# Performance work log

Hardware: AMD Instinct MI355X
Metric: run time of the kernel (lower is better)

Reference implementation:

```python
import jax, jax.numpy as jnp
import numpy as np

N_NODES = 10000
N_EDGES = 100000
IN_CH = 384
PROJ = 768  # in_channels * projection_factor
N_BLOCKS = 4
OUT_CH = 128
LN_EPS = 1e-5


def _p(key, shape, fan_in):
    return jax.random.normal(key, shape, dtype=jnp.float32) * (1.0 / np.sqrt(fan_in))


def setup_inputs() -> dict:
    key = jax.random.key(0)
    ks = iter(jax.random.split(key, 64))
    x = jax.random.normal(next(ks), (N_NODES, IN_CH), dtype=jnp.float32)
    edge_index = jax.random.randint(next(ks), (2, N_EDGES), 0, N_NODES, dtype=jnp.int64)
    inp = {
        'x': x,
        'edge_index': edge_index,
        'proj_W': _p(next(ks), (PROJ, IN_CH), IN_CH),
        'proj_b': jnp.zeros((PROJ,), jnp.float32),
        'norm_w': jnp.ones((N_BLOCKS, PROJ), jnp.float32),
        'norm_b': jnp.zeros((N_BLOCKS, PROJ), jnp.float32),
        'g1_W': _p(next(ks), (N_BLOCKS, 4 * 192, PROJ), PROJ),
        'g1_as': _p(next(ks), (N_BLOCKS, 4, 192), 192),
        'g1_ad': _p(next(ks), (N_BLOCKS, 4, 192), 192),
        'g1_b': jnp.zeros((N_BLOCKS, 4 * 192), jnp.float32),
        'g2_W': _p(next(ks), (N_BLOCKS, 2 * 96, PROJ), PROJ),
        'g2_as': _p(next(ks), (N_BLOCKS, 2, 96), 96),
        'g2_ad': _p(next(ks), (N_BLOCKS, 2, 96), 96),
        'g2_b': jnp.zeros((N_BLOCKS, 2 * 96), jnp.float32),
        'uni_W': _p(next(ks), (N_BLOCKS, PROJ, 960), 960),
        'uni_b': jnp.zeros((N_BLOCKS, PROJ), jnp.float32),
        'fnorm_w': jnp.ones((PROJ,), jnp.float32),
        'fnorm_b': jnp.zeros((PROJ,), jnp.float32),
        'fg_W': _p(next(ks), (8 * OUT_CH, PROJ), PROJ),
        'fg_as': _p(next(ks), (8, OUT_CH), OUT_CH),
        'fg_ad': _p(next(ks), (8, OUT_CH), OUT_CH),
        'fg_b': jnp.zeros((OUT_CH,), jnp.float32),
    }
    return inp


def layer_norm(x, w, b):
    m = x.mean(-1, keepdims=True)
    v = ((x - m) ** 2).mean(-1, keepdims=True)
    return (x - m) / jnp.sqrt(v + LN_EPS) * w + b


def gat_conv(x, src, dst, W, a_src, a_dst, bias, heads, out_ch, concat):
    # PyG GATConv (eval mode, add_self_loops already applied in src/dst).
    n = x.shape[0]
    h = (x @ W.T).reshape(n, heads, out_ch)          # [N,H,C]
    al_s = jnp.einsum('nhc,hc->nh', h, a_src)        # [N,H]
    al_d = jnp.einsum('nhc,hc->nh', h, a_dst)
    e = jax.nn.leaky_relu(al_s[src] + al_d[dst], 0.2)  # [E,H]
    emax = jax.ops.segment_max(e, dst, num_segments=n)
    ee = jnp.exp(e - emax[dst])
    den = jax.ops.segment_sum(ee, dst, num_segments=n)
    alpha = ee / (den[dst] + 1e-16)                  # softmax over incoming edges
    out = jax.ops.segment_sum(h[src] * alpha[:, :, None], dst, num_segments=n)
    out = out.reshape(n, heads * out_ch) if concat else out.mean(axis=1)
    return out + bias


def reference(x, edge_index, proj_W, proj_b, norm_w, norm_b,
              g1_W, g1_as, g1_ad, g1_b, g2_W, g2_as, g2_ad, g2_b,
              uni_W, uni_b, fnorm_w, fnorm_b, fg_W, fg_as, fg_ad, fg_b):
    n = x.shape[0]
    loop = jnp.arange(n, dtype=edge_index.dtype)
    src = jnp.concatenate([edge_index[0], loop])  # add self loops (PyG default)
    dst = jnp.concatenate([edge_index[1], loop])

    h = jax.nn.elu(x @ proj_W.T + proj_b)
    for i in range(N_BLOCKS):
        res = h
        hn = layer_norm(h, norm_w[i], norm_b[i])
        o1 = gat_conv(hn, src, dst, g1_W[i], g1_as[i], g1_ad[i], g1_b[i], 4, 192, True)
        o2 = gat_conv(hn, src, dst, g2_W[i], g2_as[i], g2_ad[i], g2_b[i], 2, 96, True)
        cat = jax.nn.elu(jnp.concatenate([o1, o2], axis=-1))  # [N,960]
        h = jax.nn.elu(res + cat @ uni_W[i].T + uni_b[i])
    h = layer_norm(h, fnorm_w, fnorm_b)
    return gat_conv(h, src, dst, fg_W, fg_as, fg_ad, fg_b, 8, OUT_CH, False)
```

## Files before the change

### kernel.cpp

```cpp
#include <hip/hip_runtime.h>
#include <math.h>

#define N_NODES 10000
#define N_EDGES 100000
#define E_TOT   (N_EDGES + N_NODES)
#define PROJ    768
#define LN_EPS  1e-5f

typedef __attribute__((ext_vector_type(8))) short bf16x8;
typedef __attribute__((ext_vector_type(4))) short bf16x4;
typedef __attribute__((ext_vector_type(4))) float f32x4;

__device__ __forceinline__ float elu_f(float x){ return x > 0.f ? x : __expf(x) - 1.f; }
__device__ __forceinline__ float bf2f(unsigned short u){ return __uint_as_float(((unsigned int)u) << 16); }
__device__ __forceinline__ unsigned short f2bf(float f){
  unsigned int u = __float_as_uint(f);
  return (unsigned short)((u + 0x7FFFu + ((u >> 16) & 1u)) >> 16);
}

#define GLOAD16(gp, lp) __builtin_amdgcn_global_load_lds((const __attribute__((address_space(1))) void*)(gp), (__attribute__((address_space(3))) void*)(lp), 16, 0, 0)

__global__ void k_count(const int* __restrict__ ei, int* __restrict__ cnt){
  int e = blockIdx.x*blockDim.x + threadIdx.x;
  if (e >= E_TOT) return;
  int dst = (e < N_EDGES) ? ei[N_EDGES + e] : (e - N_EDGES);
  atomicAdd(&cnt[dst], 1);
}

__global__ void k_scan(const int* __restrict__ cnt, int* __restrict__ indptr, int* __restrict__ pos){
  __shared__ int s[1024];
  __shared__ int s_running;
  int t = threadIdx.x;
  if (t == 0) s_running = 0;
  __syncthreads();
  for (int base = 0; base < N_NODES; base += 1024){
    int v = (base + t < N_NODES) ? cnt[base + t] : 0;
    s[t] = v; __syncthreads();
    for (int off = 1; off < 1024; off <<= 1){
      int add = (t >= off) ? s[t - off] : 0;
      __syncthreads();
      s[t] += add;
      __syncthreads();
    }
    int total = s[1023];
    int run = s_running;
    if (base + t < N_NODES){
      int val = run + s[t] - v;
      indptr[base + t] = val;
      pos[base + t] = val;
    }
    __syncthreads();
    if (t == 0) s_running = run + total;
    __syncthreads();
  }
  if (t == 0) indptr[N_NODES] = s_running;
}

__global__ void k_fill(const int* __restrict__ ei, int* __restrict__ pos,
                       int* __restrict__ csr_src){
  int e = blockIdx.x*blockDim.x + threadIdx.x;
  if (e >= E_TOT) return;
  int s, d;
  if (e < N_EDGES){ s = ei[e]; d = ei[N_EDGES + e]; }
  else            { s = d = e - N_EDGES; }
  int p = atomicAdd(&pos[d], 1);
  csr_src[p] = s;
}

__global__ void k_f2bf_multi(const float4* __restrict__ s0, ushort4* __restrict__ d0, int n0,
                             const float4* __restrict__ s1, ushort4* __restrict__ d1, int n1,
                             const float4* __restrict__ s2, ushort4* __restrict__ d2, int n2,
                             const float4* __restrict__ s3, ushort4* __restrict__ d3, int n3){
  int i = blockIdx.x*blockDim.x + threadIdx.x;
  const float4* src; ushort4* dst; int idx;
  if (i < n0){ src = s0; dst = d0; idx = i; }
  else if (i < n0+n1){ src = s1; dst = d1; idx = i-n0; }
  else if (i < n0+n1+n2){ src = s2; dst = d2; idx = i-n0-n1; }
  else if (i < n0+n1+n2+n3){ src = s3; dst = d3; idx = i-n0-n1-n2; }
  else return;
  float4 v = src[idx];
  ushort4 o;
  o.x = f2bf(v.x); o.y = f2bf(v.y); o.z = f2bf(v.z); o.w = f2bf(v.w);
  dst[idx] = o;
}

__global__ void k_pack_l1l2(const float* __restrict__ g1, const float* __restrict__ g2,
                            unsigned short* __restrict__ dst){
  int i = blockIdx.x*blockDim.x + threadIdx.x;
  if (i >= 737280) return;
  int layer = i / 184320;
  int off4  = i - layer*184320;
  float4 v;
  if (off4 < 147456) v = *((const float4*)(g1 + (size_t)layer*589824) + off4);
  else               v = *((const float4*)(g2 + (size_t)layer*147456) + (off4 - 147456));
  ushort4 o;
  o.x = f2bf(v.x); o.y = f2bf(v.y); o.z = f2bf(v.z); o.w = f2bf(v.w);
  ((ushort4*)(dst + (size_t)layer*737280))[off4] = o;
}

__global__ void k_layernorm_bf(const unsigned short* __restrict__ x, const float* __restrict__ w,
                               const float* __restrict__ b, unsigned short* __restrict__ y){
  int n = blockIdx.x;
  int t = threadIdx.x;
  const unsigned short* xr = x + (size_t)n*PROJ;
  float v0=0.f, v1=0.f, v2=0.f, v3=0.f;
  if (t < 192){
    bf16x4 hv = *(const bf16x4*)(xr + t*4);
    v0 = bf2f((unsigned short)hv.x); v1 = bf2f((unsigned short)hv.y);
    v2 = bf2f((unsigned short)hv.z); v3 = bf2f((unsigned short)hv.w);
  }
  float s  = v0+v1+v2+v3;
  float s2 = v0*v0 + v1*v1 + v2*v2 + v3*v3;
  #pragma unroll
  for (int off = 32; off; off >>= 1){ s += __shfl_down(s, off); s2 += __shfl_down(s2, off); }
  __shared__ float rs[4], rs2[4];
  __shared__ float s_mean, s_rstd;
  int wid = t >> 6, lane = t & 63;
  if (lane == 0){ rs[wid] = s; rs2[wid] = s2; }
  __syncthreads();
  if (t == 0){
    float S  = rs[0]+rs[1]+rs[2]+rs[3];
    float S2 = rs2[0]+rs2[1]+rs2[2]+rs2[3];
    float m  = S * (1.f/768.f);
    float var = S2 * (1.f/768.f) - m*m;
    s_mean = m; s_rstd = rsqrtf(var + LN_EPS);
  }
  __syncthreads();
  if (t < 192){
    float m = s_mean, r = s_rstd;
    float4 wv = *(const float4*)&w[t*4];
    float4 bv = *(const float4*)&b[t*4];
    ushort4 o;
    o.x = f2bf((v0-m)*r*wv.x + bv.x);
    o.y = f2bf((v1-m)*r*wv.y + bv.y);
    o.z = f2bf((v2-m)*r*wv.z + bv.z);
    o.w = f2bf((v3-m)*r*wv.w + bv.w);
    *(ushort4*)(y + (size_t)n*PROJ + t*4) = o;
  }
}

template<int EPI>
__global__ __launch_bounds__(256, 8)
void k_gemm_mfma(const unsigned short* __restrict__ A, int lda,
                 const unsigned short* __restrict__ W,
                 unsigned short* __restrict__ C, int ldc,
                 int M, int N, int K,
                 const float* __restrict__ bias,
                 const unsigned short* __restrict__ res, int ldres, int NBN){
  __shared__ unsigned short As[3][128*32];
  __shared__ unsigned short Bs[3][64*32];
  const int tid = threadIdx.x;
  const int lane = tid & 63, wid = tid >> 6;
  const int wm = wid >> 1, wn = wid & 1;

  const int nwg = gridDim.x;
  const int q = nwg >> 3, r = nwg & 7;
  const int xcd = blockIdx.x & 7, o = blockIdx.x >> 3;
  const int swz = (xcd < r ? xcd*(q+1) : r*(q+1) + (xcd - r)*q) + o;
  const int bm = (swz / NBN) * 128;
  const int bn = (swz % NBN) * 64;

  const int srow = tid >> 2;
  const int sc   = (tid & 3) ^ ((tid >> 3) & 3);
  size_t ga0 = (size_t)min(bm + srow,      M-1)*lda + sc*8;
  size_t ga1 = (size_t)min(bm + 64 + srow, M-1)*lda + sc*8;
  size_t gb0 = (size_t)min(bn + srow,      N-1)*K   + sc*8;
  const int ldst = tid*8;

  f32x4 acc[4][2];
  #pragma unroll
  for (int i=0;i<4;i++)
    #pragma unroll
    for (int j=0;j<2;j++) acc[i][j] = (f32x4){0.f,0.f,0.f,0.f};

  const int rA = wm*64 + (lane & 15);
  const int rB = wn*32 + (lane & 15);
  const int cu = (((lane >> 4)) ^ (((lane & 15) >> 1) & 3)) * 8;

  const int NT = K >> 5;
  int bcur = 0;
  GLOAD16(A + ga0, &As[0][ldst]);
  GLOAD16(A + ga1, &As[0][2048 + ldst]);
  GLOAD16(W + gb0, &Bs[0][ldst]);

  for (int t = 0; t < NT; ++t){
    if (t + 1 < NT){
      int bst = bcur + 1; if (bst == 3) bst = 0;
      const int k0 = (t+1) << 5;
      GLOAD16(A + ga0 + k0, &As[bst][ldst]);
      GLOAD16(A + ga1 + k0, &As[bst][2048 + ldst]);
      GLOAD16(W + gb0 + k0, &Bs[bst][ldst]);
      asm volatile("s_waitcnt vmcnt(3)" ::: "memory");
    } else {
      asm volatile("s_waitcnt vmcnt(0)" ::: "memory");
    }
    __builtin_amdgcn_sched_barrier(0);
    __builtin_amdgcn_s_barrier();
    __builtin_amdgcn_sched_barrier(0);

    bf16x8 af[4], bfr[2];
    #pragma unroll
    for (int mi = 0; mi < 4; mi++)
      af[mi] = *(const bf16x8*)&As[bcur][(rA + mi*16)*32 + cu];
    #pragma unroll
    for (int ni = 0; ni < 2; ni++)
      bfr[ni] = *(const bf16x8*)&Bs[bcur][(rB + ni*16)*32 + cu];
    #pragma unroll
    for (int mi = 0; mi < 4; mi++)
      #pragma unroll
      for (int ni = 0; ni < 2; ni++)
        acc[mi][ni] = __builtin_amdgcn_mfma_f32_16x16x32_bf16(af[mi], bfr[ni], acc[mi][ni], 0,0,0);

    bcur += 1; if (bcur == 3) bcur = 0;
  }

  const int mrow0 = bm + wm*64 + ((lane>>4)<<2);
  const int ncol0 = bn + wn*32 + (lane & 15);
  #pragma unroll
  for (int mi=0; mi<4; mi++){
    #pragma unroll
    for (int rr=0; rr<4; rr++){
      int m = mrow0 + mi*16 + rr;
      if (m >= M) continue;
      #pragma unroll
      for (int ni=0; ni<2; ni++){
        int n = ncol0 + ni*16;
        float v = acc[mi][ni][rr];
        if (EPI == 1){
          v = elu_f(v + bias[n]);
        } else if (EPI == 2){
          v = elu_f(v + bias[n] + bf2f(res[(size_t)m*ldres + n]));
        }
        C[(size_t)m*ldc + n] = f2bf(v);
      }
    }
  }
}

__global__ void k_attn_coef6(const unsigned short* __restrict__ hlin,
                             const float* __restrict__ as1, const float* __restrict__ ad1,
                             const float* __restrict__ as2, const float* __restrict__ ad2,
                             float* __restrict__ als, float* __restrict__ ald){
  int n = blockIdx.x;
  int wid = threadIdx.x >> 6, lane = threadIdx.x & 63;
  int C    = wid < 4 ? 192 : 96;
  int base = wid < 4 ? wid*192 : 768 + (wid-4)*96;
  const float* as_ = wid < 4 ? as1 + wid*192 : as2 + (wid-4)*96;
  const float* ad_ = wid < 4 ? ad1 + wid*192 : ad2 + (wid-4)*96;
  float ss = 0.f, sd = 0.f;
  if (lane*4 < C){
    bf16x4 hv = *(const bf16x4*)(hlin + (size_t)n*960 + base + lane*4);
    float4 a1 = *(const float4*)&as_[lane*4];
    float4 a2 = *(const float4*)&ad_[lane*4];
    float h0 = bf2f((unsigned short)hv.x), h1 = bf2f((unsigned short)hv.y);
    float h2 = bf2f((unsigned short)hv.z), h3 = bf2f((unsigned short)hv.w);
    ss = h0*a1.x + h1*a1.y + h2*a1.z + h3*a1.w;
    sd = h0*a2.x + h1*a2.y + h2*a2.z + h3*a2.w;
  }
  #pragma unroll
  for (int off = 32; off; off >>= 1){ ss += __shfl_down(ss, off); sd += __shfl_down(sd, off); }
  if (lane == 0){ als[n*6 + wid] = ss; ald[n*6 + wid] = sd; }
}

__global__ void k_attn_coef8(const unsigned short* __restrict__ hlin,
                             const float* __restrict__ a_src, const float* __restrict__ a_dst,
                             float* __restrict__ als, float* __restrict__ ald){
  int n = blockIdx.x;
  int wid = threadIdx.x >> 6, lane = threadIdx.x & 63;
  float ss = 0.f, sd = 0.f;
  if (lane < 32){
    bf16x4 hv = *(const bf16x4*)(hlin + (size_t)n*1024 + wid*128 + lane*4);
    float4 a1 = *(const float4*)&a_src[wid*128 + lane*4];
    float4 a2 = *(const float4*)&a_dst[wid*128 + lane*4];
    float h0 = bf2f((unsigned short)hv.x), h1 = bf2f((unsigned short)hv.y);
    float h2 = bf2f((unsigned short)hv.z), h3 = bf2f((unsigned short)hv.w);
    ss = h0*a1.x + h1*a1.y + h2*a1.z + h3*a1.w;
    sd = h0*a2.x + h1*a2.y + h2*a2.z + h3*a2.w;
  }
  #pragma unroll
  for (int off = 32; off; off >>= 1){ ss += __shfl_down(ss, off); sd += __shfl_down(sd, off); }
  if (lane == 0){ als[n*8 + wid] = ss; ald[n*8 + wid] = sd; }
}

template<int MODE>
__global__ __launch_bounds__(256)
void k_attn_fused(const unsigned short* __restrict__ hlin, int ldh,
                  const float* __restrict__ als, const float* __restrict__ ald,
                  const int* __restrict__ indptr, const int* __restrict__ csr_src,
                  const float* __restrict__ b1, const float* __restrict__ b2,
                  void* __restrict__ outv, int ldo){
  constexpr int TOT = MODE ? 1024 : 960;
  constexpr int HT  = MODE ? 8 : 6;
  constexpr int CH8 = TOT/8;
  constexpr int CPL = (CH8 + 63)/64;
  int n = blockIdx.x;
  int tid = threadIdx.x;
  int wv = tid >> 6, lane = tid & 63;
  int beg = indptr[n], end = indptr[n+1], deg = end - beg;

  __shared__ float s_m[HT], s_dinv[HT], s_ald[HT];
  __shared__ float s_alpha[64*HT];
  __shared__ int   s_src[64];
  __shared__ float s_red[4][TOT];

  for (int h = wv; h < HT; h += 4){
    float aldv = ald[n*HT + h];
    float m = -1e30f, d = 0.f;
    for (int e = beg + lane; e < end; e += 64){
      int s = csr_src[e];
      float v = als[s*HT + h] + aldv;
      v = v > 0.f ? v : 0.2f*v;
      if (v > m){ d *= __expf(m - v); m = v; }
      d += __expf(v - m);
    }
    #pragma unroll
    for (int off = 1; off < 64; off <<= 1){
      float mo_ = __shfl_xor(m, off);
      float dd  = __shfl_xor(d, off);
      float mn  = fmaxf(m, mo_);
      d = d*__expf(m - mn) + dd*__expf(mo_ - mn);
      m = mn;
    }
    if (lane == 0){ s_m[h] = m; s_dinv[h] = 1.f/(d + 1e-16f); s_ald[h] = aldv; }
  }

  int hof[CPL];
  #pragma unroll
  for (int p = 0; p < CPL; p++){
    int idx = (lane + p*64)*8;
    hof[p] = MODE ? (idx >> 7) : (idx < 768 ? idx/192 : 4 + (idx-768)/96);
  }

  f32x4 accA[CPL], accB[CPL];
  #pragma unroll
  for (int p = 0; p < CPL; p++){ accA[p] = (f32x4){0,0,0,0}; accB[p] = (f32x4){0,0,0,0}; }

  for (int base = 0; base < deg; base += 64){
    int chunk = min(64, deg - base);
    __syncthreads();
    if (tid < chunk) s_src[tid] = csr_src[beg + base + tid];
    __syncthreads();
    for (int i = tid; i < chunk*HT; i += 256){
      int e = i / HT, h = i - e*HT;
      float v = als[s_src[e]*HT + h] + s_ald[h];
      v = v > 0.f ? v : 0.2f*v;
      s_alpha[e*HT + h] = __expf(v - s_m[h]) * s_dinv[h];
    }
    __syncthreads();

    int e = wv;
    for (; e + 4 < chunk; e += 8){
      int s0 = s_src[e], s1 = s_src[e+4];
      const bf16x8* hr0 = (const bf16x8*)(hlin + (size_t)s0*ldh);
      const bf16x8* hr1 = (const bf16x8*)(hlin + (size_t)s1*ldh);
      const float* ae0 = &s_alpha[e*HT];
      const float* ae1 = &s_alpha[(e+4)*HT];
      bf16x8 hv0[CPL], hv1[CPL];
      #pragma unroll
      for (int p = 0; p < CPL; p++){
        int ch = lane + p*64;
        if (CH8 % 64 == 0 || ch < CH8){ hv0[p] = hr0[ch]; hv1[p] = hr1[ch]; }
      }
      #pragma unroll
      for (int p = 0; p < CPL; p++){
        int ch = lane + p*64;
        if (CH8 % 64 == 0 || ch < CH8){
          float a0 = ae0[hof[p]], a1 = ae1[hof[p]];
          accA[p].x += bf2f((unsigned short)hv0[p][0])*a0 + bf2f((unsigned short)hv1[p][0])*a1;
          accA[p].y += bf2f((unsigned short)hv0[p][1])*a0 + bf2f((unsigned short)hv1[p][1])*a1;
          accA[p].z += bf2f((unsigned short)hv0[p][2])*a0 + bf2f((unsigned short)hv1[p][2])*a1;
          accA[p].w += bf2f((unsigned short)hv0[p][3])*a0 + bf2f((unsigned short)hv1[p][3])*a1;
          accB[p].x += bf2f((unsigned short)hv0[p][4])*a0 + bf2f((unsigned short)hv1[p][4])*a1;
          accB[p].y += bf2f((unsigned short)hv0[p][5])*a0 + bf2f((unsigned short)hv1[p][5])*a1;
          accB[p].z += bf2f((unsigned short)hv0[p][6])*a0 + bf2f((unsigned short)hv1[p][6])*a1;
          accB[p].w += bf2f((unsigned short)hv0[p][7])*a0 + bf2f((unsigned short)hv1[p][7])*a1;
        }
      }
    }
    for (; e < chunk; e += 4){
      int s = s_src[e];
      const bf16x8* hr = (const bf16x8*)(hlin + (size_t)s*ldh);
      const float* ae = &s_alpha[e*HT];
      #pragma unroll
      for (int p = 0; p < CPL; p++){
        int ch = lane + p*64;
        if (CH8 % 64 == 0 || ch < CH8){
          float al = ae[hof[p]];
          bf16x8 hv = hr[ch];
          accA[p].x += bf2f((unsigned short)hv[0])*al;
          accA[p].y += bf2f((unsigned short)hv[1])*al;
          accA[p].z += bf2f((unsigned short)hv[2])*al;
          accA[p].w += bf2f((unsigned short)hv[3])*al;
          accB[p].x += bf2f((unsigned short)hv[4])*al;
          accB[p].y += bf2f((unsigned short)hv[5])*al;
          accB[p].z += bf2f((unsigned short)hv[6])*al;
          accB[p].w += bf2f((unsigned short)hv[7])*al;
        }
      }
    }
  }

  #pragma unroll
  for (int p = 0; p < CPL; p++){
    int ch = lane + p*64;
    if (CH8 % 64 == 0 || ch < CH8){
      *(f32x4*)&s_red[wv][ch*8]     = accA[p];
      *(f32x4*)&s_red[wv][ch*8 + 4] = accB[p];
    }
  }
  __syncthreads();

  if (MODE == 0){
    unsigned short* out = (unsigned short*)outv;
    #pragma unroll
    for (int qq = 0; qq < 4; qq++){
      int idx = tid + qq*256;
      if (idx < TOT){
        float bb = idx < 768 ? b1[idx] : b2[idx - 768];
        float v = s_red[0][idx] + s_red[1][idx] + s_red[2][idx] + s_red[3][idx] + bb;
        out[(size_t)n*ldo + idx] = f2bf(elu_f(v));
      }
    }
  } else {
    float* out = (float*)outv;
    if (tid < 128){
      float v = 0.f;
      #pragma unroll
      for (int h = 0; h < 8; h++){
        int idx = h*128 + tid;
        v += s_red[0][idx] + s_red[1][idx] + s_red[2][idx] + s_red[3][idx];
      }
      out[(size_t)n*ldo + tid] = v*0.125f + b1[tid];
    }
  }
}

extern "C" void kernel_launch(void* const* d_in, const int* in_sizes, int n_in,
                              void* d_out, int out_size, void* d_ws, size_t ws_size,
                              hipStream_t stream){
  const float* x      = (const float*)d_in[0];
  const int*   ei     = (const int*)  d_in[1];
  const float* proj_W = (const float*)d_in[2];
  const float* proj_b = (const float*)d_in[3];
  const float* norm_w = (const float*)d_in[4];
  const float* norm_b = (const float*)d_in[5];
  const float* g1_W   = (const float*)d_in[6];
  const float* g1_as  = (const float*)d_in[7];
  const float* g1_ad  = (const float*)d_in[8];
  const float* g1_b   = (const float*)d_in[9];
  const float* g2_W   = (const float*)d_in[10];
  const float* g2_as  = (const float*)d_in[11];
  const float* g2_ad  = (const float*)d_in[12];
  const float* g2_b   = (const float*)d_in[13];
  const float* uni_W  = (const float*)d_in[14];
  const float* uni_b  = (const float*)d_in[15];
  const float* fnorm_w= (const float*)d_in[16];
  const float* fnorm_b= (const float*)d_in[17];
  const float* fg_W   = (const float*)d_in[18];
  const float* fg_as  = (const float*)d_in[19];
  const float* fg_ad  = (const float*)d_in[20];
  const float* fg_b   = (const float*)d_in[21];

  float* w = (float*)d_ws;
  unsigned short* h  = (unsigned short*)w; w += 3840000;
  unsigned short* h2 = (unsigned short*)w; w += 3840000;
  unsigned short* linbuf = (unsigned short*)w; w += 5120000;
  unsigned short* hnb  = (unsigned short*)w; w += 3840000;
  unsigned short* catb = (unsigned short*)w; w += 4800000;
  unsigned short* wb   = (unsigned short*)w; w += 3489792;
  float* als   = w; w += 80000;
  float* ald   = w; w += 80000;
  int* iw = (int*)w;
  int* cnt     = iw; iw += 10016;
  int* indptr  = iw; iw += 10016;
  int* pos     = iw; iw += 10016;
  int* csr_src = iw; iw += 110016;

  unsigned short* wb_proj = wb;
  unsigned short* wb_l12  = wb_proj + 294912;
  unsigned short* wb_uni  = wb_l12 + 2949120;
  unsigned short* wb_fg   = wb_uni + 2949120;

  hipMemsetAsync(cnt, 0, N_NODES*sizeof(int), stream);
  k_count<<<(E_TOT+255)/256, 256, 0, stream>>>(ei, cnt);
  k_scan<<<1, 1024, 0, stream>>>(cnt, indptr, pos);
  k_fill<<<(E_TOT+255)/256, 256, 0, stream>>>(ei, pos, csr_src);

  k_f2bf_multi<<<(1967616+255)/256, 256, 0, stream>>>(
      (const float4*)x, (ushort4*)hnb, 960000,
      (const float4*)proj_W, (ushort4*)wb_proj, 73728,
      (const float4*)uni_W, (ushort4*)wb_uni, 737280,
      (const float4*)fg_W, (ushort4*)wb_fg, 196608);
  k_pack_l1l2<<<(737280+255)/256, 256, 0, stream>>>(g1_W, g2_W, wb_l12);

  dim3 blk(256);

  k_gemm_mfma<1><<<dim3(79*12), blk, 0, stream>>>(hnb, 384, wb_proj, h, 768, N_NODES, 768, 384, proj_b, nullptr, 0, 12);

  unsigned short* cur = h;
  unsigned short* oth = h2;
  for (int i = 0; i < 4; i++){
    k_layernorm_bf<<<N_NODES, 256, 0, stream>>>(cur, norm_w + i*768, norm_b + i*768, hnb);
    k_gemm_mfma<0><<<dim3(79*15), blk, 0, stream>>>(hnb, 768, wb_l12 + (size_t)i*737280, linbuf, 960, N_NODES, 960, 768, nullptr, nullptr, 0, 15);
    k_attn_coef6<<<N_NODES, 384, 0, stream>>>(linbuf, g1_as + i*768, g1_ad + i*768, g2_as + i*192, g2_ad + i*192, als, ald);
    k_attn_fused<0><<<N_NODES, 256, 0, stream>>>(linbuf, 960, als, ald, indptr, csr_src, g1_b + i*768, g2_b + i*192, catb, 960);
    k_gemm_mfma<2><<<dim3(79*12), blk, 0, stream>>>(catb, 960, wb_uni + (size_t)i*737280, oth, 768, N_NODES, 768, 960, uni_b + i*768, cur, 768, 12);
    unsigned short* t = cur; cur = oth; oth = t;
  }

  k_layernorm_bf<<<N_NODES, 256, 0, stream>>>(cur, fnorm_w, fnorm_b, hnb);
  k_gemm_mfma<0><<<dim3(79*16), blk, 0, stream>>>(hnb, 768, wb_fg, linbuf, 1024, N_NODES, 1024, 768, nullptr, nullptr, 0, 16);
  k_attn_coef8<<<N_NODES, 512, 0, stream>>>(linbuf, fg_as, fg_ad, als, ald);
  k_attn_fused<1><<<N_NODES, 256, 0, stream>>>(linbuf, 1024, als, ald, indptr, csr_src, fg_b, nullptr, d_out, 128);
}
```

Baseline: 699.0 us.

## Process one node per wavefront in GAT attention aggregation, removing block syncs

The attention aggregation kernel now assigns one destination node to each 64-lane wavefront (4 nodes per block) instead of one node per 256-thread block. Softmax statistics for all heads are computed in registers by the wave. Per-edge alphas are computed by the first HT lanes and broadcast with shuffles, which removes the shared-memory staging, the __syncthreads barriers and the cross-wave reduction. The trade-off is fewer edges in flight per node and narrower 4-element bf16 loads per lane, where the old kernel used 8-element loads.

New measurement: 716.3 us. 1.02x slower.

```diff
diff --git a/kernel.cpp b/kernel.cpp
--- a/kernel.cpp
+++ b/kernel.cpp
@@ -284,154 +284,139 @@
 
 template<int MODE>
 __global__ __launch_bounds__(256)
-void k_attn_fused(const unsigned short* __restrict__ hlin, int ldh,
-                  const float* __restrict__ als, const float* __restrict__ ald,
-                  const int* __restrict__ indptr, const int* __restrict__ csr_src,
-                  const float* __restrict__ b1, const float* __restrict__ b2,
-                  void* __restrict__ outv, int ldo){
+void k_attn_node(const unsigned short* __restrict__ hlin, int ldh,
+                 const float* __restrict__ als, const float* __restrict__ ald,
+                 const int* __restrict__ indptr, const int* __restrict__ csr_src,
+                 const float* __restrict__ b1, const float* __restrict__ b2,
+                 void* __restrict__ outv, int ldo){
   constexpr int TOT = MODE ? 1024 : 960;
   constexpr int HT  = MODE ? 8 : 6;
-  constexpr int CH8 = TOT/8;
-  constexpr int CPL = (CH8 + 63)/64;
-  int n = blockIdx.x;
-  int tid = threadIdx.x;
-  int wv = tid >> 6, lane = tid & 63;
-  int beg = indptr[n], end = indptr[n+1], deg = end - beg;
-
-  __shared__ float s_m[HT], s_dinv[HT], s_ald[HT];
-  __shared__ float s_alpha[64*HT];
-  __shared__ int   s_src[64];
-  __shared__ float s_red[4][TOT];
-
-  for (int h = wv; h < HT; h += 4){
-    float aldv = ald[n*HT + h];
-    float m = -1e30f, d = 0.f;
-    for (int e = beg + lane; e < end; e += 64){
-      int s = csr_src[e];
-      float v = als[s*HT + h] + aldv;
+  __shared__ float s_scr[4][MODE ? 1024 : 1];
+
+  int wv = threadIdx.x >> 6, lane = threadIdx.x & 63;
+  int n = blockIdx.x*4 + wv;
+  if (n >= N_NODES) return;
+  int beg = indptr[n], end = indptr[n+1];
+
+  float m[HT], d[HT], aldv[HT];
+  #pragma unroll
+  for (int h = 0; h < HT; h++){ m[h] = -1e30f; d[h] = 0.f; aldv[h] = ald[n*HT + h]; }
+  for (int e = beg + lane; e < end; e += 64){
+    int s = csr_src[e];
+    #pragma unroll
+    for (int h = 0; h < HT; h++){
+      float v = als[s*HT + h] + aldv[h];
       v = v > 0.f ? v : 0.2f*v;
-      if (v > m){ d *= __expf(m - v); m = v; }
-      d += __expf(v - m);
-    }
-    #pragma unroll
-    for (int off = 1; off < 64; off <<= 1){
-      float mo_ = __shfl_xor(m, off);
-      float dd  = __shfl_xor(d, off);
-      float mn  = fmaxf(m, mo_);
-      d = d*__expf(m - mn) + dd*__expf(mo_ - mn);
-      m = mn;
-    }
-    if (lane == 0){ s_m[h] = m; s_dinv[h] = 1.f/(d + 1e-16f); s_ald[h] = aldv; }
-  }
-
-  int hof[CPL];
-  #pragma unroll
-  for (int p = 0; p < CPL; p++){
-    int idx = (lane + p*64)*8;
+      if (v > m[h]){ d[h] *= __expf(m[h] - v); m[h] = v; }
+      d[h] += __expf(v - m[h]);
+    }
+  }
+  #pragma unroll
+  for (int off = 1; off < 64; off <<= 1){
+    #pragma unroll
+    for (int h = 0; h < HT; h++){
+      float mo = __shfl_xor(m[h], off);
+      float dd = __shfl_xor(d[h], off);
+      float mn = fmaxf(m[h], mo);
+      d[h] = d[h]*__expf(m[h] - mn) + dd*__expf(mo - mn);
+      m[h] = mn;
+    }
+  }
+  float mh = m[0], dh = 1.f/(d[0] + 1e-16f), av = aldv[0];
+  #pragma unroll
+  for (int h = 1; h < HT; h++){
+    if (lane == h){ mh = m[h]; dh = 1.f/(d[h] + 1e-16f); av = aldv[h]; }
+  }
+
+  int hof[4];
+  #pragma unroll
+  for (int p = 0; p < 4; p++){
+    int idx = (p*64 + lane)*4;
     hof[p] = MODE ? (idx >> 7) : (idx < 768 ? idx/192 : 4 + (idx-768)/96);
   }
 
-  f32x4 accA[CPL], accB[CPL];
-  #pragma unroll
-  for (int p = 0; p < CPL; p++){ accA[p] = (f32x4){0,0,0,0}; accB[p] = (f32x4){0,0,0,0}; }
-
-  for (int base = 0; base < deg; base += 64){
-    int chunk = min(64, deg - base);
-    __syncthreads();
-    if (tid < chunk) s_src[tid] = csr_src[beg + base + tid];
-    __syncthreads();
-    for (int i = tid; i < chunk*HT; i += 256){
-      int e = i / HT, h = i - e*HT;
-      float v = als[s_src[e]*HT + h] + s_ald[h];
-      v = v > 0.f ? v : 0.2f*v;
-      s_alpha[e*HT + h] = __expf(v - s_m[h]) * s_dinv[h];
-    }
-    __syncthreads();
-
-    int e = wv;
-    for (; e + 4 < chunk; e += 8){
-      int s0 = s_src[e], s1 = s_src[e+4];
-      const bf16x8* hr0 = (const bf16x8*)(hlin + (size_t)s0*ldh);
-      const bf16x8* hr1 = (const bf16x8*)(hlin + (size_t)s1*ldh);
-      const float* ae0 = &s_alpha[e*HT];
-      const float* ae1 = &s_alpha[(e+4)*HT];
-      bf16x8 hv0[CPL], hv1[CPL];
-      #pragma unroll
-      for (int p = 0; p < CPL; p++){
-        int ch = lane + p*64;
-        if (CH8 % 64 == 0 || ch < CH8){ hv0[p] = hr0[ch]; hv1[p] = hr1[ch]; }
+  f32x4 acc[4];
+  #pragma unroll
+  for (int p = 0; p < 4; p++) acc[p] = (f32x4){0.f,0.f,0.f,0.f};
+
+  int e = beg;
+  for (; e + 1 < end; e += 2){
+    int s0 = csr_src[e], s1 = csr_src[e+1];
+    float al0 = 0.f, al1 = 0.f;
+    if (lane < HT){
+      float v0 = als[s0*HT + lane] + av; v0 = v0 > 0.f ? v0 : 0.2f*v0;
+      al0 = __expf(v0 - mh)*dh;
+      float v1 = als[s1*HT + lane] + av; v1 = v1 > 0.f ? v1 : 0.2f*v1;
+      al1 = __expf(v1 - mh)*dh;
+    }
+    const bf16x4* r0 = (const bf16x4*)(hlin + (size_t)s0*ldh);
+    const bf16x4* r1 = (const bf16x4*)(hlin + (size_t)s1*ldh);
+    #pragma unroll
+    for (int p = 0; p < 4; p++){
+      int ch = p*64 + lane;
+      if (TOT == 1024 || ch*4 < TOT){
+        bf16x4 h0 = r0[ch], h1 = r1[ch];
+        float a0 = __shfl(al0, hof[p]);
+        float a1 = __shfl(al1, hof[p]);
+        acc[p].x += bf2f((unsigned short)h0.x)*a0 + bf2f((unsigned short)h1.x)*a1;
+        acc[p].y += bf2f((unsigned short)h0.y)*a0 + bf2f((unsigned short)h1.y)*a1;
+        acc[p].z += bf2f((unsigned short)h0.z)*a0 + bf2f((unsigned short)h1.z)*a1;
+        acc[p].w += bf2f((unsigned short)h0.w)*a0 + bf2f((unsigned short)h1.w)*a1;
       }
-      #pragma unroll
-      for (int p = 0; p < CPL; p++){
-        int ch = lane + p*64;
-        if (CH8 % 64 == 0 || ch < CH8){
-          float a0 = ae0[hof[p]], a1 = ae1[hof[p]];
-          accA[p].x += bf2f((unsigned short)hv0[p][0])*a0 + bf2f((unsigned short)hv1[p][0])*a1;
-          accA[p].y += bf2f((unsigned short)hv0[p][1])*a0 + bf2f((unsigned short)hv1[p][1])*a1;
-          accA[p].z += bf2f((unsigned short)hv0[p][2])*a0 + bf2f((unsigned short)hv1[p][2])*a1;
-          accA[p].w += bf2f((unsigned short)hv0[p][3])*a0 + bf2f((unsigned short)hv1[p][3])*a1;
-          accB[p].x += bf2f((unsigned short)hv0[p][4])*a0 + bf2f((unsigned short)hv1[p][4])*a1;
-          accB[p].y += bf2f((unsigned short)hv0[p][5])*a0 + bf2f((unsigned short)hv1[p][5])*a1;
-          accB[p].z += bf2f((unsigned short)hv0[p][6])*a0 + bf2f((unsigned short)hv1[p][6])*a1;
-          accB[p].w += bf2f((unsigned short)hv0[p][7])*a0 + bf2f((unsigned short)hv1[p][7])*a1;
-        }
+    }
+  }
+  for (; e < end; e++){
+    int s0 = csr_src[e];
+    float al0 = 0.f;
+    if (lane < HT){
+      float v0 = als[s0*HT + lane] + av; v0 = v0 > 0.f ? v0 : 0.2f*v0;
+      al0 = __expf(v0 - mh)*dh;
+    }
+    const bf16x4* r0 = (const bf16x4*)(hlin + (size_t)s0*ldh);
+    #pragma unroll
+    for (int p = 0; p < 4; p++){
+      int ch = p*64 + lane;
+      if (TOT == 1024 || ch*4 < TOT){
+        bf16x4 h0 = r0[ch];
+        float a0 = __shfl(al0, hof[p]);
+        acc[p].x += bf2f((unsigned short)h0.x)*a0;
+        acc[p].y += bf2f((unsigned short)h0.y)*a0;
+        acc[p].z += bf2f((unsigned short)h0.z)*a0;
+        acc[p].w += bf2f((unsigned short)h0.w)*a0;
       }
     }
-    for (; e < chunk; e += 4){
-      int s = s_src[e];
-      const bf16x8* hr = (const bf16x8*)(hlin + (size_t)s*ldh);
-      const float* ae = &s_alpha[e*HT];
-      #pragma unroll
-      for (int p = 0; p < CPL; p++){
-        int ch = lane + p*64;
-        if (CH8 % 64 == 0 || ch < CH8){
-          float al = ae[hof[p]];
-          bf16x8 hv = hr[ch];
-          accA[p].x += bf2f((unsigned short)hv[0])*al;
-          accA[p].y += bf2f((unsigned short)hv[1])*al;
-          accA[p].z += bf2f((unsigned short)hv[2])*al;
-          accA[p].w += bf2f((unsigned short)hv[3])*al;
-          accB[p].x += bf2f((unsigned short)hv[4])*al;
-          accB[p].y += bf2f((unsigned short)hv[5])*al;
-          accB[p].z += bf2f((unsigned short)hv[6])*al;
-          accB[p].w += bf2f((unsigned short)hv[7])*al;
-        }
-      }
-    }
-  }
-
-  #pragma unroll
-  for (int p = 0; p < CPL; p++){
-    int ch = lane + p*64;
-    if (CH8 % 64 == 0 || ch < CH8){
-      *(f32x4*)&s_red[wv][ch*8]     = accA[p];
-      *(f32x4*)&s_red[wv][ch*8 + 4] = accB[p];
-    }
-  }
-  __syncthreads();
+  }
 
   if (MODE == 0){
     unsigned short* out = (unsigned short*)outv;
     #pragma unroll
-    for (int qq = 0; qq < 4; qq++){
-      int idx = tid + qq*256;
+    for (int p = 0; p < 4; p++){
+      int idx = (p*64 + lane)*4;
       if (idx < TOT){
-        float bb = idx < 768 ? b1[idx] : b2[idx - 768];
-        float v = s_red[0][idx] + s_red[1][idx] + s_red[2][idx] + s_red[3][idx] + bb;
-        out[(size_t)n*ldo + idx] = f2bf(elu_f(v));
+        const float* bb = idx < 768 ? &b1[idx] : &b2[idx - 768];
+        float4 bv = *(const float4*)bb;
+        ushort4 o;
+        o.x = f2bf(elu_f(acc[p].x + bv.x));
+        o.y = f2bf(elu_f(acc[p].y + bv.y));
+        o.z = f2bf(elu_f(acc[p].z + bv.z));
+        o.w = f2bf(elu_f(acc[p].w + bv.w));
+        *(ushort4*)(out + (size_t)n*ldo + idx) = o;
       }
     }
   } else {
+    #pragma unroll
+    for (int p = 0; p < 4; p++)
+      *(f32x4*)&s_scr[wv][(p*64 + lane)*4] = acc[p];
     float* out = (float*)outv;
-    if (tid < 128){
-      float v = 0.f;
-      #pragma unroll
-      for (int h = 0; h < 8; h++){
-        int idx = h*128 + tid;
-        v += s_red[0][idx] + s_red[1][idx] + s_red[2][idx] + s_red[3][idx];
-      }
-      out[(size_t)n*ldo + tid] = v*0.125f + b1[tid];
-    }
+    int c0 = lane*2, c1 = lane*2 + 1;
+    float o0 = 0.f, o1 = 0.f;
+    #pragma unroll
+    for (int h = 0; h < 8; h++){
+      o0 += s_scr[wv][h*128 + c0];
+      o1 += s_scr[wv][h*128 + c1];
+    }
+    out[(size_t)n*ldo + c0] = o0*0.125f + b1[c0];
+    out[(size_t)n*ldo + c1] = o1*0.125f + b1[c1];
   }
 }
 
@@ -503,7 +488,7 @@
     k_layernorm_bf<<<N_NODES, 256, 0, stream>>>(cur, norm_w + i*768, norm_b + i*768, hnb);
     k_gemm_mfma<0><<<dim3(79*15), blk, 0, stream>>>(hnb, 768, wb_l12 + (size_t)i*737280, linbuf, 960, N_NODES, 960, 768, nullptr, nullptr, 0, 15);
     k_attn_coef6<<<N_NODES, 384, 0, stream>>>(linbuf, g1_as + i*768, g1_ad + i*768, g2_as + i*192, g2_ad + i*192, als, ald);
-    k_attn_fused<0><<<N_NODES, 256, 0, stream>>>(linbuf, 960, als, ald, indptr, csr_src, g1_b + i*768, g2_b + i*192, catb, 960);
+    k_attn_node<0><<<dim3(2500), blk, 0, stream>>>(linbuf, 960, als, ald, indptr, csr_src, g1_b + i*768, g2_b + i*192, catb, 960);
     k_gemm_mfma<2><<<dim3(79*12), blk, 0, stream>>>(catb, 960, wb_uni + (size_t)i*737280, oth, 768, N_NODES, 768, 960, uni_b + i*768, cur, 768, 12);
     unsigned short* t = cur; cur = oth; oth = t;
   }
@@ -511,5 +496,5 @@
   k_layernorm_bf<<<N_NODES, 256, 0, stream>>>(cur, fnorm_w, fnorm_b, hnb);
   k_gemm_mfma<0><<<dim3(79*16), blk, 0, stream>>>(hnb, 768, wb_fg, linbuf, 1024, N_NODES, 1024, 768, nullptr, nullptr, 0, 16);
   k_attn_coef8<<<N_NODES, 512, 0, stream>>>(linbuf, fg_as, fg_ad, als, ald);
-  k_attn_fused<1><<<N_NODES, 256, 0, stream>>>(linbuf, 1024, als, ald, indptr, csr_src, fg_b, nullptr, d_out, 128);
-}
+  k_attn_node<1><<<dim3(2500), blk, 0, stream>>>(linbuf, 1024, als, ald, indptr, csr_src, fg_b, nullptr, d_out, 128);
+}
```
